# Performance work log

Hardware: AMD Instinct MI355X
Metric: run time of the kernel (lower is better)

Reference implementation:

```python
import jax, jax.numpy as jnp
import numpy as np

DEPTH_MIN = 0.0
DEPTH_MAX = 1.0
NUM_BINS = 64
LOSS_WEIGHT = 1.0
EPS = 1e-12  # torch F.normalize default eps


def setup_inputs() -> dict:
    key = jax.random.key(0)
    k1, k2, k3 = jax.random.split(key, 3)
    N, C, H, W = 4, 256, 128, 160
    preds_S = jax.random.normal(k1, (N, C, H, W), jnp.float32)
    preds_T = jax.random.normal(k2, (N, C, H, W), jnp.float32)
    depth_gt_resized = jax.random.uniform(k3, (N, 1, H, W), jnp.float32)
    return {"preds_S": preds_S, "preds_T": preds_T, "depth_gt_resized": depth_gt_resized}


def _bin_indices_ud(depth):
    # Uniform discretization (mode='UD'), target=True clamping semantics
    bin_size = (DEPTH_MAX - DEPTH_MIN) / NUM_BINS
    idx = (depth - DEPTH_MIN) / bin_size
    invalid = (idx < 0) | (idx > NUM_BINS) | ~jnp.isfinite(idx)
    idx = jnp.where(invalid, NUM_BINS, idx)
    return idx.astype(jnp.int32)  # truncation toward zero, matches torch int64 cast for >=0 values


def _protos(feats, idx):
    # feats: (P, C) pixel features; idx: (P,) bin ids in [0, NUM_BINS]
    # segment mean per bin, then L2-normalize along channels -> (NUM_BINS, C)
    sums = jax.ops.segment_sum(feats, idx, num_segments=NUM_BINS + 1)
    counts = jax.ops.segment_sum(jnp.ones(idx.shape, feats.dtype), idx, num_segments=NUM_BINS + 1)
    means = sums[:NUM_BINS] / jnp.maximum(counts[:NUM_BINS, None], 1.0)
    norm = jnp.linalg.norm(means, axis=1, keepdims=True)
    return means / jnp.maximum(norm, EPS)


def reference(preds_S, preds_T, depth_gt_resized):
    N, C, H, W = preds_S.shape
    idx = _bin_indices_ud(depth_gt_resized[:, 0]).reshape(-1)  # (N*H*W,)
    # pixels-major layout: (N, H, W, C) -> (P, C)
    fS = preds_S.transpose(0, 2, 3, 1).reshape(-1, C)
    fT = preds_T.transpose(0, 2, 3, 1).reshape(-1, C)
    pS = _protos(fS, idx)  # (bins, C)
    pT = _protos(fT, idx)
    sim_S = pS @ pS.T  # (bins, bins)
    sim_T = pT @ pT.T
    return LOSS_WEIGHT * jnp.mean((sim_S - sim_T) ** 2)
```

## Files before the change

### kernel.cpp

```cpp
#include <hip/hip_runtime.h>

#define NB     64
#define CCH    256
#define HW     20480
#define TPB    512
#define NTILE  4
#define GRID_MS 1280

#define WS_COUNTS 262144
#define WS_ACC    262404
#define WS_TICKET 262408
#define WS_ZERO   262412
#define REP_STRIDE (2 * NB * CCH)
#define WS_PS     131072
#define WS_PT     196608

typedef __attribute__((ext_vector_type(8))) short short8;
typedef __attribute__((ext_vector_type(4))) float f32x4;

#define STRIDE 136

__global__ __launch_bounds__(256, 8)
void k_msum(const float* __restrict__ predsS,
            const float* __restrict__ predsT,
            const float* __restrict__ depth,
            float* __restrict__ sums,
            int* __restrict__ counts) {
    int tid = threadIdx.x;
    int blk = blockIdx.x;
    int prange = blk % 40;
    int group  = blk / 40;
    int tensor = group >> 4;
    int n  = (group >> 2) & 3;
    int cs = group & 3;
    int px0 = prange * TPB;

    const float* xbase = (tensor ? predsT : predsS)
                       + (size_t)(n * CCH + cs * 64) * HW + px0;
    const float* dbase = depth + n * HW + px0;

    __shared__ short sHi[64][STRIDE];
    __shared__ unsigned char sBin[TPB];
    __shared__ int lhist[NB + 1];

    bool desig = (tensor == 0) && (cs == 0);
    if (desig && tid < NB + 1) lhist[tid] = 0;
    __syncthreads();

    for (int i = tid; i < TPB; i += 256) {
        float f = dbase[i] * 64.0f;
        int b;
        if (!(f >= 0.0f) || f > 64.0f) b = NB;
        else b = (int)f;
        sBin[i] = (unsigned char)b;
        if (desig) atomicAdd(&lhist[b], 1);
    }

    int lane = tid & 63;
    int wv = tid >> 6;
    int l15 = lane & 15;
    int q = lane >> 4;
    int r0 = tid >> 5;
    int c0 = tid & 31;

    f32x4 acc[4];
    #pragma unroll
    for (int mt = 0; mt < 4; ++mt) acc[mt] = (f32x4)0.0f;

    for (int tt = 0; tt < NTILE; ++tt) {
        int t0 = tt * 128;
        float4 vv[8];
        #pragma unroll
        for (int rr = 0; rr < 8; ++rr)
            vv[rr] = *(const float4*)(xbase + (size_t)(rr * 8 + r0) * HW + t0 + c0 * 4);
        __syncthreads();
        #pragma unroll
        for (int rr = 0; rr < 8; ++rr) {
            unsigned u0 = __float_as_uint(vv[rr].x), u1 = __float_as_uint(vv[rr].y);
            unsigned u2 = __float_as_uint(vv[rr].z), u3 = __float_as_uint(vv[rr].w);
            uint2 hv;
            hv.x = ((u0 + 0x8000u) >> 16) | ((u1 + 0x8000u) & 0xFFFF0000u);
            hv.y = ((u2 + 0x8000u) >> 16) | ((u3 + 0x8000u) & 0xFFFF0000u);
            *(uint2*)&sHi[rr * 8 + r0][c0 * 4] = hv;
        }
        __syncthreads();
        #pragma unroll
        for (int ks = 0; ks < 4; ++ks) {
            unsigned long long bv = *(const unsigned long long*)&sBin[t0 + ks * 32 + q * 8];
            short8 bHi = *(const short8*)&sHi[wv * 16 + l15][ks * 32 + q * 8];
            #pragma unroll
            for (int mt = 0; mt < 4; ++mt) {
                int tgt = mt * 16 + l15;
                short8 afr;
                #pragma unroll
                for (int j = 0; j < 8; ++j)
                    afr[j] = ((int)((bv >> (8 * j)) & 0xFFull) == tgt) ? (short)0x3F80 : (short)0;
                acc[mt] = __builtin_amdgcn_mfma_f32_16x16x32_bf16(afr, bHi, acc[mt], 0, 0, 0);
            }
        }
    }
    float* dst = sums + (size_t)(blk & 1) * REP_STRIDE
               + (size_t)tensor * NB * CCH + cs * 64 + wv * 16 + l15;
    #pragma unroll
    for (int mt = 0; mt < 4; ++mt)
        #pragma unroll
        for (int r = 0; r < 4; ++r)
            atomicAdd(&dst[(mt * 16 + q * 4 + r) * CCH], acc[mt][r]);
    if (desig) {
        __syncthreads();
        if (tid < NB + 1 && lhist[tid] != 0) atomicAdd(&counts[tid], lhist[tid]);
    }
}

__global__ __launch_bounds__(256) void k_protos(const float* __restrict__ sums,
                                                const int* __restrict__ counts,
                                                float* __restrict__ pS,
                                                float* __restrict__ pT) {
    int b = blockIdx.x, t = threadIdx.x;
    int ci = counts[b];
    float cnt = (float)(ci < 1 ? 1 : ci);
    float mS = (sums[b * CCH + t] + sums[REP_STRIDE + b * CCH + t]) / cnt;
    float mT = (sums[(NB + b) * CCH + t] + sums[REP_STRIDE + (NB + b) * CCH + t]) / cnt;
    float ss = mS * mS, st = mT * mT;
    #pragma unroll
    for (int o = 32; o; o >>= 1) {
        ss += __shfl_xor(ss, o, 64);
        st += __shfl_xor(st, o, 64);
    }
    __shared__ float rs[4], rt[4];
    int w = t >> 6;
    if ((t & 63) == 0) { rs[w] = ss; rt[w] = st; }
    __syncthreads();
    float nS = sqrtf(rs[0] + rs[1] + rs[2] + rs[3]);
    float nT = sqrtf(rt[0] + rt[1] + rt[2] + rt[3]);
    pS[b * CCH + t] = mS / fmaxf(nS, 1e-12f);
    pT[b * CCH + t] = mT / fmaxf(nT, 1e-12f);
}

__global__ __launch_bounds__(256) void k_sim(const float* __restrict__ pS,
                                             const float* __restrict__ pT,
                                             float* __restrict__ acc,
                                             unsigned int* __restrict__ ticket,
                                             float* __restrict__ out) {
    int i = blockIdx.x;
    int t = threadIdx.x;
    int j = t & 63, seg = t >> 6;
    __shared__ float rowS[CCH], rowT[CCH];
    rowS[t] = pS[i * CCH + t];
    rowT[t] = pT[i * CCH + t];
    __syncthreads();
    const float4* Sj = (const float4*)(pS + j * CCH + seg * 64);
    const float4* Tj = (const float4*)(pT + j * CCH + seg * 64);
    const float4* Si = (const float4*)(rowS + seg * 64);
    const float4* Ti = (const float4*)(rowT + seg * 64);
    float dS = 0.0f, dT = 0.0f;
    #pragma unroll
    for (int k = 0; k < 16; ++k) {
        float4 a = Si[k], b = Sj[k];
        dS += a.x * b.x + a.y * b.y + a.z * b.z + a.w * b.w;
        float4 c = Ti[k], d = Tj[k];
        dT += c.x * d.x + c.y * d.y + c.z * d.z + c.w * d.w;
    }
    __shared__ float sS[4][64], sT[4][64];
    sS[seg][j] = dS;
    sT[seg][j] = dT;
    __syncthreads();
    if (t < 64) {
        float fS = sS[0][t] + sS[1][t] + sS[2][t] + sS[3][t];
        float fT = sT[0][t] + sT[1][t] + sT[2][t] + sT[3][t];
        float e = fS - fT;
        e = e * e;
        #pragma unroll
        for (int o = 32; o; o >>= 1) e += __shfl_xor(e, o, 64);
        if (t == 0) {
            atomicAdd(acc, e);
            __threadfence();
            unsigned int r = atomicAdd(ticket, 1u);
            if (r == NB - 1) {
                float tot = atomicAdd(acc, 0.0f);
                out[0] = tot * (1.0f / (float)(NB * NB));
            }
        }
    }
}

extern "C" void kernel_launch(void* const* d_in, const int* in_sizes, int n_in,
                              void* d_out, int out_size, void* d_ws, size_t ws_size,
                              hipStream_t stream) {
    const float* predsS = (const float*)d_in[0];
    const float* predsT = (const float*)d_in[1];
    const float* depth  = (const float*)d_in[2];
    char* ws = (char*)d_ws;
    float* sums = (float*)ws;
    int* counts = (int*)(ws + WS_COUNTS);
    float* acc = (float*)(ws + WS_ACC);
    unsigned int* ticket = (unsigned int*)(ws + WS_TICKET);
    float* pS = (float*)(ws + WS_PS);
    float* pT = (float*)(ws + WS_PT);

    hipMemsetAsync(ws, 0, WS_ZERO, stream);
    k_msum<<<GRID_MS, 256, 0, stream>>>(predsS, predsT, depth, sums, counts);
    k_protos<<<NB, 256, 0, stream>>>(sums, counts, pS, pT);
    k_sim<<<NB, 256, 0, stream>>>(pS, pT, acc, ticket, (float*)d_out);
}
```

Baseline: 210.0 us.

## Retile segment-sum kernel to 16 channels by 1024 pixels with in-block reduction

The binned segment-sum kernel changes its block tile from 64 channels by 512 pixels to 16 channels by 1024 pixels. Each wave now covers a distinct pixel slice rather than a distinct channel slice. The four waves' MFMA accumulators are reduced through shared memory before the global atomic adds, so each block issues a quarter as many atomics. The second tile's global loads are issued before the first tile's MFMA work, giving some load/compute overlap. In exchange the grid has more blocks (2560 vs 1280), the bin index array is recomputed for more channel groups, and the occupancy hint drops to 6 blocks per CU.

Result: faster. 202.7 us (-3.5%).

```diff
diff --git a/kernel.cpp b/kernel.cpp
--- a/kernel.cpp
+++ b/kernel.cpp
@@ -3,24 +3,24 @@
 #define NB     64
 #define CCH    256
 #define HW     20480
-#define TPB    512
-#define NTILE  4
-#define GRID_MS 1280
-
+#define PXB    1024
+#define NPR    (HW/PXB)
+#define GRID_MS (2*4*16*NPR)
+
+#define REP_STRIDE (2 * NB * CCH)
 #define WS_COUNTS 262144
 #define WS_ACC    262404
 #define WS_TICKET 262408
 #define WS_ZERO   262412
-#define REP_STRIDE (2 * NB * CCH)
 #define WS_PS     131072
 #define WS_PT     196608
 
 typedef __attribute__((ext_vector_type(8))) short short8;
 typedef __attribute__((ext_vector_type(4))) float f32x4;
 
-#define STRIDE 136
-
-__global__ __launch_bounds__(256, 8)
+#define ROWSTR 520
+
+__global__ __launch_bounds__(256, 6)
 void k_msum(const float* __restrict__ predsS,
             const float* __restrict__ predsT,
             const float* __restrict__ depth,
@@ -28,26 +28,26 @@
             int* __restrict__ counts) {
     int tid = threadIdx.x;
     int blk = blockIdx.x;
-    int prange = blk % 40;
-    int group  = blk / 40;
-    int tensor = group >> 4;
-    int n  = (group >> 2) & 3;
-    int cs = group & 3;
-    int px0 = prange * TPB;
+    int prange = blk % NPR;
+    int group  = blk / NPR;
+    int tensor = group >> 6;
+    int n  = (group >> 4) & 3;
+    int cg = group & 15;
+    int px0 = prange * PXB;
 
     const float* xbase = (tensor ? predsT : predsS)
-                       + (size_t)(n * CCH + cs * 64) * HW + px0;
+                       + (size_t)(n * CCH + cg * 16) * HW + px0;
     const float* dbase = depth + n * HW + px0;
 
-    __shared__ short sHi[64][STRIDE];
-    __shared__ unsigned char sBin[TPB];
+    __shared__ short sHi[16][ROWSTR];
+    __shared__ unsigned char sBin[PXB];
     __shared__ int lhist[NB + 1];
 
-    bool desig = (tensor == 0) && (cs == 0);
+    bool desig = (tensor == 0) && (cg == 0);
     if (desig && tid < NB + 1) lhist[tid] = 0;
     __syncthreads();
 
-    for (int i = tid; i < TPB; i += 256) {
+    for (int i = tid; i < PXB; i += 256) {
         float f = dbase[i] * 64.0f;
         int b;
         if (!(f >= 0.0f) || f > 64.0f) b = NB;
@@ -56,38 +56,45 @@
         if (desig) atomicAdd(&lhist[b], 1);
     }
 
-    int lane = tid & 63;
-    int wv = tid >> 6;
-    int l15 = lane & 15;
-    int q = lane >> 4;
-    int r0 = tid >> 5;
-    int c0 = tid & 31;
+    int lane = tid & 63, wv = tid >> 6;
+    int l15 = lane & 15, q = lane >> 4;
 
     f32x4 acc[4];
     #pragma unroll
     for (int mt = 0; mt < 4; ++mt) acc[mt] = (f32x4)0.0f;
 
-    for (int tt = 0; tt < NTILE; ++tt) {
-        int t0 = tt * 128;
-        float4 vv[8];
-        #pragma unroll
-        for (int rr = 0; rr < 8; ++rr)
-            vv[rr] = *(const float4*)(xbase + (size_t)(rr * 8 + r0) * HW + t0 + c0 * 4);
+    float4 vv[8];
+    #pragma unroll
+    for (int i = 0; i < 8; ++i) {
+        int rr = i >> 1, p2 = i & 1;
+        vv[i] = *(const float4*)(xbase + (size_t)(wv * 4 + rr) * HW + p2 * 256 + lane * 4);
+    }
+
+    for (int tt = 0; tt < 2; ++tt) {
         __syncthreads();
         #pragma unroll
-        for (int rr = 0; rr < 8; ++rr) {
-            unsigned u0 = __float_as_uint(vv[rr].x), u1 = __float_as_uint(vv[rr].y);
-            unsigned u2 = __float_as_uint(vv[rr].z), u3 = __float_as_uint(vv[rr].w);
+        for (int i = 0; i < 8; ++i) {
+            int rr = i >> 1, p2 = i & 1;
+            unsigned u0 = __float_as_uint(vv[i].x), u1 = __float_as_uint(vv[i].y);
+            unsigned u2 = __float_as_uint(vv[i].z), u3 = __float_as_uint(vv[i].w);
             uint2 hv;
             hv.x = ((u0 + 0x8000u) >> 16) | ((u1 + 0x8000u) & 0xFFFF0000u);
             hv.y = ((u2 + 0x8000u) >> 16) | ((u3 + 0x8000u) & 0xFFFF0000u);
-            *(uint2*)&sHi[rr * 8 + r0][c0 * 4] = hv;
+            *(uint2*)&sHi[wv * 4 + rr][p2 * 256 + lane * 4] = hv;
+        }
+        if (tt == 0) {
+            #pragma unroll
+            for (int i = 0; i < 8; ++i) {
+                int rr = i >> 1, p2 = i & 1;
+                vv[i] = *(const float4*)(xbase + (size_t)(wv * 4 + rr) * HW + 512 + p2 * 256 + lane * 4);
+            }
         }
         __syncthreads();
+        int pbase = tt * 512 + wv * 128;
         #pragma unroll
         for (int ks = 0; ks < 4; ++ks) {
-            unsigned long long bv = *(const unsigned long long*)&sBin[t0 + ks * 32 + q * 8];
-            short8 bHi = *(const short8*)&sHi[wv * 16 + l15][ks * 32 + q * 8];
+            unsigned long long bv = *(const unsigned long long*)&sBin[pbase + ks * 32 + q * 8];
+            short8 bHi = *(const short8*)&sHi[l15][wv * 128 + ks * 32 + q * 8];
             #pragma unroll
             for (int mt = 0; mt < 4; ++mt) {
                 int tgt = mt * 16 + l15;
@@ -99,17 +106,24 @@
             }
         }
     }
+
+    __syncthreads();
+    float* red = (float*)&sHi[0][0];
+    #pragma unroll
+    for (int mt = 0; mt < 4; ++mt)
+        #pragma unroll
+        for (int r = 0; r < 4; ++r)
+            red[wv * 1024 + (mt * 16 + q * 4 + r) * 16 + l15] = acc[mt][r];
+    __syncthreads();
     float* dst = sums + (size_t)(blk & 1) * REP_STRIDE
-               + (size_t)tensor * NB * CCH + cs * 64 + wv * 16 + l15;
-    #pragma unroll
-    for (int mt = 0; mt < 4; ++mt)
-        #pragma unroll
-        for (int r = 0; r < 4; ++r)
-            atomicAdd(&dst[(mt * 16 + q * 4 + r) * CCH], acc[mt][r]);
-    if (desig) {
-        __syncthreads();
-        if (tid < NB + 1 && lhist[tid] != 0) atomicAdd(&counts[tid], lhist[tid]);
-    }
+               + (size_t)tensor * NB * CCH + cg * 16;
+    #pragma unroll
+    for (int k = 0; k < 4; ++k) {
+        int e = tid + k * 256;
+        float s = red[e] + red[1024 + e] + red[2048 + e] + red[3072 + e];
+        atomicAdd(&dst[(e >> 4) * CCH + (e & 15)], s);
+    }
+    if (desig && tid < NB + 1 && lhist[tid] != 0) atomicAdd(&counts[tid], lhist[tid]);
 }
 
 __global__ __launch_bounds__(256) void k_protos(const float* __restrict__ sums,
```
